# Performance work log

Hardware: AMD Instinct MI355X
Metric: run time of the kernel (lower is better)

The kernel has to match this reference:

```python
import jax, jax.numpy as jnp
import numpy as np

N_NODES = 100000


def gcn_conv(x, W, b, src, dst, num_nodes):
    """PyG GCNConv: add self-loops, symmetric deg^{-1/2} normalization,
    linear transform, scatter-add aggregation (source -> target), bias."""
    h = x @ W  # [N, out]
    # degree on target nodes, counting the added self-loop (+1)
    deg = jax.ops.segment_sum(jnp.ones_like(dst, dtype=h.dtype), dst,
                              num_segments=num_nodes) + 1.0
    dinv = jax.lax.rsqrt(deg)  # deg >= 1 always
    norm = dinv[src] * dinv[dst]  # [E]
    agg = jax.ops.segment_sum(h[src] * norm[:, None], dst,
                              num_segments=num_nodes)
    # self-loop contribution: norm_ii = dinv[i]^2
    out = agg + h * (dinv * dinv)[:, None]
    return out + b


def setup_inputs() -> dict:
    key = jax.random.key(0)
    ks = jax.random.split(key, 8)
    num_features, hidden, emb = 64, 64, 32
    x = jax.random.normal(ks[0], (N_NODES, num_features), dtype=jnp.float32)
    edge_index = jax.random.randint(ks[1], (2, 1600000), 0, N_NODES, dtype=jnp.int64)
    def glorot(k, shape):
        lim = float(np.sqrt(6.0 / (shape[0] + shape[1])))
        return jax.random.uniform(k, shape, jnp.float32, -lim, lim)
    return {
        "x": x,
        "edge_index": edge_index,
        "W1": glorot(ks[2], (num_features, hidden)),
        "b1": jnp.zeros((hidden,), jnp.float32),
        "W2": glorot(ks[3], (hidden, hidden)),
        "b2": jnp.zeros((hidden,), jnp.float32),
        "Wf": glorot(ks[4], (hidden, emb)),
        "bf": jnp.zeros((emb,), jnp.float32),
    }


def reference(x, edge_index, W1, b1, W2, b2, Wf, bf):
    src, dst = edge_index[0], edge_index[1]
    n = x.shape[0]
    h = gcn_conv(x, W1, b1, src, dst, n)
    h = jax.nn.relu(h)  # dropout is identity in eval mode
    h = gcn_conv(h, W2, b2, src, dst, n)
    h = jax.nn.relu(h)
    return h @ Wf + bf
```

## Files before the change

### kernel.cpp

```cpp
#include <hip/hip_runtime.h>


#define NODE_SHIFT 8
#define NODES_PER_BKT 256
#define BKT_CAP 5120
#define CSR_CAP 7168
#define NB_PART 256
#define HPAD 68

__device__ __forceinline__ unsigned short f2bf_rne(float f) {
    unsigned int u = __float_as_uint(f);
    unsigned int r = (u + 0x7FFFu + ((u >> 16) & 1u)) >> 16;
    return (unsigned short)r;
}
__device__ __forceinline__ float bf_lo(unsigned int u) {
    return __uint_as_float(u << 16);
}
__device__ __forceinline__ float bf_hi(unsigned int u) {
    return __uint_as_float(u & 0xFFFF0000u);
}

__global__ __launch_bounds__(256) void partition_kernel(const int* __restrict__ src,
                                                        const int* __restrict__ dst, int E,
                                                        int* __restrict__ bkt_cursor,
                                                        unsigned int* __restrict__ staging,
                                                        int K1, int CHK) {
    __shared__ int lcnt[400];
    __shared__ int lcur[400];
    const int tid = threadIdx.x;
    const int start = blockIdx.x * CHK;
    const int end = min(E, start + CHK);
    for (int k = tid; k < 400; k += 256) lcnt[k] = 0;
    __syncthreads();
    const int s4 = start >> 2;
    const int e4 = end >> 2;
    for (int i = s4 + tid; i < e4; i += 256) {
        const int4 d = ((const int4*)dst)[i];
        atomicAdd(&lcnt[d.x >> NODE_SHIFT], 1);
        atomicAdd(&lcnt[d.y >> NODE_SHIFT], 1);
        atomicAdd(&lcnt[d.z >> NODE_SHIFT], 1);
        atomicAdd(&lcnt[d.w >> NODE_SHIFT], 1);
    }
    __syncthreads();
    for (int k = tid; k < K1; k += 256) {
        int c = lcnt[k];
        int g = c ? atomicAdd(&bkt_cursor[k], c) : 0;
        lcur[k] = k * BKT_CAP + g;
    }
    __syncthreads();
    for (int i = s4 + tid; i < e4; i += 256) {
        const int4 d = ((const int4*)dst)[i];
        const int4 s = ((const int4*)src)[i];
        int pos;
        pos = atomicAdd(&lcur[d.x >> NODE_SHIFT], 1);
        staging[pos] = ((unsigned int)(d.x & (NODES_PER_BKT - 1)) << 17) | (unsigned int)s.x;
        pos = atomicAdd(&lcur[d.y >> NODE_SHIFT], 1);
        staging[pos] = ((unsigned int)(d.y & (NODES_PER_BKT - 1)) << 17) | (unsigned int)s.y;
        pos = atomicAdd(&lcur[d.z >> NODE_SHIFT], 1);
        staging[pos] = ((unsigned int)(d.z & (NODES_PER_BKT - 1)) << 17) | (unsigned int)s.z;
        pos = atomicAdd(&lcur[d.w >> NODE_SHIFT], 1);
        staging[pos] = ((unsigned int)(d.w & (NODES_PER_BKT - 1)) << 17) | (unsigned int)s.w;
    }
}

__global__ __launch_bounds__(256) void bucket_build_kernel(const unsigned int* __restrict__ staging,
                                                           const int* __restrict__ bkt_cursor,
                                                           float* __restrict__ dinv,
                                                           int* __restrict__ offs,
                                                           int* __restrict__ n_e,
                                                           int* __restrict__ csr_src,
                                                           int N) {
    __shared__ int cnt[NODES_PER_BKT];
    __shared__ int wsum[4];
    const int tid = threadIdx.x;
    const int node0 = blockIdx.x * NODES_PER_BKT;
    const int estart = blockIdx.x * BKT_CAP;
    const int eend = estart + bkt_cursor[blockIdx.x];
    const int cstart = blockIdx.x * CSR_CAP;

    cnt[tid] = 0;
    __syncthreads();
    for (int e = estart + tid; e < eend; e += 256)
        atomicAdd(&cnt[staging[e] >> 17], 1);
    __syncthreads();

    const int lane = tid & 63;
    const int wave = tid >> 6;
    const int c = cnt[tid];
    const int cp = (c + 7) & ~7;
    int inc = cp;
#pragma unroll
    for (int o = 1; o < 64; o <<= 1) {
        int t = __shfl_up(inc, o, 64);
        if (lane >= o) inc += t;
    }
    if (lane == 63) wsum[wave] = inc;
    __syncthreads();
    int wpre = 0;
#pragma unroll
    for (int w = 0; w < 4; w++) wpre += (w < wave) ? wsum[w] : 0;
    const int p = cstart + wpre + inc - cp;

    const int node = node0 + tid;
    __syncthreads();
    if (node < N) {
        offs[node] = p;
        n_e[node] = cp;
        dinv[node] = rsqrtf((float)c + 1.0f);
    }
    cnt[tid] = p;
    __syncthreads();
    for (int e = estart + tid; e < eend; e += 256) {
        const unsigned int r = staging[e];
        int pos = atomicAdd(&cnt[r >> 17], 1);
        csr_src[pos] = (int)(r & 0x1FFFFu);
    }
    for (int j = c; j < cp; j++) csr_src[p + j] = N;
}

__global__ __launch_bounds__(256) void gemm1_kernel(const float* __restrict__ X,
                                                    const float* __restrict__ W,
                                                    const float* __restrict__ dinv,
                                                    unsigned short* __restrict__ Y, int N) {
    constexpr int OUTC = 64, RPT = 8;
    constexpr int R = 128;
    constexpr int RPAD = R + (R / 32) * 4;
    __shared__ float Ws[64 * OUTC];
    __shared__ float Xt[64 * RPAD];

    const int tid = threadIdx.x;
    const int row0 = blockIdx.x * R;

    for (int l = tid; l < 64 * OUTC / 4; l += 256)
        ((float4*)Ws)[l] = ((const float4*)W)[l];

    for (int l = tid; l < R * 16; l += 256) {
        const int r = l & (R - 1);
        const int kq = l >> 7;
        float4 v = make_float4(0.f, 0.f, 0.f, 0.f);
        const int row = row0 + r;
        if (row < N) v = ((const float4*)(X + (long)row * 64))[kq];
        const int rp = r + (r >> 5) * 4;
        Xt[(4 * kq + 0) * RPAD + rp] = v.x;
        Xt[(4 * kq + 1) * RPAD + rp] = v.y;
        Xt[(4 * kq + 2) * RPAD + rp] = v.z;
        Xt[(4 * kq + 3) * RPAD + rp] = v.w;
    }
    __syncthreads();

    const int cg = tid % 16;
    const int rg = tid / 16;
    const int c0 = cg * 4;
    const int r0 = rg * RPT;
    const int r0p = r0 + (r0 >> 5) * 4;

    float acc[RPT][4];
#pragma unroll
    for (int i = 0; i < RPT; i++)
#pragma unroll
        for (int j = 0; j < 4; j++) acc[i][j] = 0.f;

#pragma unroll 4
    for (int k = 0; k < 64; k++) {
        float xv[RPT];
        const float4 xa = *(const float4*)&Xt[k * RPAD + r0p];
        const float4 xb = *(const float4*)&Xt[k * RPAD + r0p + 4];
        xv[0] = xa.x; xv[1] = xa.y; xv[2] = xa.z; xv[3] = xa.w;
        xv[4] = xb.x; xv[5] = xb.y; xv[6] = xb.z; xv[7] = xb.w;
        const float4 wa = *(const float4*)&Ws[k * OUTC + c0];
        const float wv[4] = {wa.x, wa.y, wa.z, wa.w};
#pragma unroll
        for (int i = 0; i < RPT; i++)
#pragma unroll
            for (int j = 0; j < 4; j++)
                acc[i][j] += xv[i] * wv[j];
    }

#pragma unroll
    for (int i = 0; i < RPT; i++) {
        const int row = row0 + r0 + i;
        if (row < N) {
            const float sc = dinv[row];
            ushort4 o16;
            o16.x = f2bf_rne(acc[i][0] * sc);
            o16.y = f2bf_rne(acc[i][1] * sc);
            o16.z = f2bf_rne(acc[i][2] * sc);
            o16.w = f2bf_rne(acc[i][3] * sc);
            *(ushort4*)&Y[(long)row * OUTC + c0] = o16;
        }
    }
}

template <int OUTC, bool HEAD>
__global__ __launch_bounds__(256) void fused_agg_gemm_kernel(
    const unsigned short* __restrict__ T, const int* __restrict__ offs,
    const int* __restrict__ n_e, const int* __restrict__ csr_src,
    const float* __restrict__ dinv, const float* __restrict__ aggbias,
    const float* __restrict__ W, const float* __restrict__ headbias,
    void* __restrict__ Yv, int N) {
    __shared__ float Ws[2048];
    __shared__ float hs[32 * HPAD];

    const int tid = threadIdx.x;
    constexpr int KSPLIT = (OUTC == 64) ? 32 : 64;

    for (int l = tid; l < 512; l += 256)
        ((float4*)Ws)[l] = ((const float4*)W)[l];

    const int nl = tid >> 3;
    const int node = blockIdx.x * 32 + nl;
    const int l8 = tid & 7;
    const int fo = l8 * 8;

    float o[8];
    if (node < N) {
        const int start = offs[node];
        const int n_edges = n_e[node];
        const int* ep = csr_src + start;

        float acc[8];
#pragma unroll
        for (int j = 0; j < 8; j++) acc[j] = 0.f;

        if (n_edges > 0) {
            int4 ia = ((const int4*)ep)[0];
            int4 ib = ((const int4*)ep)[1];
            for (int e = 0; e < n_edges; e += 8) {
                uint4 h[8];
                h[0] = *(const uint4*)&T[(long)ia.x * 64 + fo];
                h[1] = *(const uint4*)&T[(long)ia.y * 64 + fo];
                h[2] = *(const uint4*)&T[(long)ia.z * 64 + fo];
                h[3] = *(const uint4*)&T[(long)ia.w * 64 + fo];
                h[4] = *(const uint4*)&T[(long)ib.x * 64 + fo];
                h[5] = *(const uint4*)&T[(long)ib.y * 64 + fo];
                h[6] = *(const uint4*)&T[(long)ib.z * 64 + fo];
                h[7] = *(const uint4*)&T[(long)ib.w * 64 + fo];
                const int next = e + 8;
                if (next < n_edges) {
                    ia = ((const int4*)(ep + next))[0];
                    ib = ((const int4*)(ep + next))[1];
                }
#pragma unroll
                for (int j = 0; j < 8; j++) {
                    acc[0] += bf_lo(h[j].x); acc[1] += bf_hi(h[j].x);
                    acc[2] += bf_lo(h[j].y); acc[3] += bf_hi(h[j].y);
                    acc[4] += bf_lo(h[j].z); acc[5] += bf_hi(h[j].z);
                    acc[6] += bf_lo(h[j].w); acc[7] += bf_hi(h[j].w);
                }
            }
        }

        const float di = dinv[node];
        const uint4 sv = *(const uint4*)&T[(long)node * 64 + fo];
        const float self[8] = {bf_lo(sv.x), bf_hi(sv.x), bf_lo(sv.y), bf_hi(sv.y),
                               bf_lo(sv.z), bf_hi(sv.z), bf_lo(sv.w), bf_hi(sv.w)};
        const float4 ba = *(const float4*)&aggbias[fo];
        const float4 bb = *(const float4*)&aggbias[fo + 4];
        const float bv[8] = {ba.x, ba.y, ba.z, ba.w, bb.x, bb.y, bb.z, bb.w};
#pragma unroll
        for (int j = 0; j < 8; j++)
            o[j] = fmaxf(di * (acc[j] + self[j]) + bv[j], 0.f);
    } else {
#pragma unroll
        for (int j = 0; j < 8; j++) o[j] = 0.f;
    }
    float* hp = &hs[nl * HPAD + fo];
    *(float4*)hp = make_float4(o[0], o[1], o[2], o[3]);
    *(float4*)(hp + 4) = make_float4(o[4], o[5], o[6], o[7]);
    __syncthreads();

    constexpr int CPT = OUTC / 8;
    const int row = blockIdx.x * 32 + (tid >> 3);
    const int c0 = (tid & 7) * CPT;
    const int lrow = tid >> 3;

    float acc2[CPT];
#pragma unroll
    for (int j = 0; j < CPT; j++) acc2[j] = 0.f;

#pragma unroll 4
    for (int k = 0; k < KSPLIT; k++) {
        const float x = hs[lrow * HPAD + k];
        const float4 wa = *(const float4*)&Ws[k * OUTC + c0];
        acc2[0] += x * wa.x;
        acc2[1] += x * wa.y;
        acc2[2] += x * wa.z;
        acc2[3] += x * wa.w;
        if (CPT == 8) {
            const float4 wb = *(const float4*)&Ws[k * OUTC + c0 + 4];
            acc2[4] += x * wb.x;
            acc2[5] += x * wb.y;
            acc2[6] += x * wb.z;
            acc2[7] += x * wb.w;
        }
    }

    if (OUTC == 64) {
        __syncthreads();
        for (int l = tid; l < 512; l += 256)
            ((float4*)Ws)[l] = ((const float4*)W)[512 + l];
        __syncthreads();
#pragma unroll 4
        for (int k = 32; k < 64; k++) {
            const float x = hs[lrow * HPAD + k];
            const float4 wa = *(const float4*)&Ws[(k - 32) * OUTC + c0];
            acc2[0] += x * wa.x;
            acc2[1] += x * wa.y;
            acc2[2] += x * wa.z;
            acc2[3] += x * wa.w;
            const float4 wb = *(const float4*)&Ws[(k - 32) * OUTC + c0 + 4];
            acc2[4] += x * wb.x;
            acc2[5] += x * wb.y;
            acc2[6] += x * wb.z;
            acc2[7] += x * wb.w;
        }
    }

    if (row < N) {
        if (HEAD) {
            const float4 hb = *(const float4*)&headbias[c0];
            float* yp = &((float*)Yv)[(long)row * OUTC + c0];
            *(float4*)yp = make_float4(acc2[0] + hb.x, acc2[1] + hb.y,
                                       acc2[2] + hb.z, acc2[3] + hb.w);
        } else {
            const float sc = dinv[row];
            unsigned short* yp = &((unsigned short*)Yv)[(long)row * OUTC + c0];
            ushort4 o0, o1;
            o0.x = f2bf_rne(acc2[0] * sc); o0.y = f2bf_rne(acc2[1] * sc);
            o0.z = f2bf_rne(acc2[2] * sc); o0.w = f2bf_rne(acc2[3] * sc);
            o1.x = f2bf_rne(acc2[4] * sc); o1.y = f2bf_rne(acc2[5] * sc);
            o1.z = f2bf_rne(acc2[6] * sc); o1.w = f2bf_rne(acc2[7] * sc);
            *(ushort4*)yp = o0;
            *(ushort4*)(yp + 4) = o1;
        }
    }
}

extern "C" void kernel_launch(void* const* d_in, const int* in_sizes, int n_in,
                              void* d_out, int out_size, void* d_ws, size_t ws_size,
                              hipStream_t stream) {
    const float* x  = (const float*)d_in[0];
    const int*   ei = (const int*)d_in[1];
    const float* W1 = (const float*)d_in[2];
    const float* b1 = (const float*)d_in[3];
    const float* W2 = (const float*)d_in[4];
    const float* b2 = (const float*)d_in[5];
    const float* Wf = (const float*)d_in[6];
    const float* bf = (const float*)d_in[7];

    const int N = in_sizes[0] / 64;
    const int E = in_sizes[1] / 2;
    const int* src = ei;
    const int* dst = ei + E;
    const int K1 = (N + NODES_PER_BKT - 1) / NODES_PER_BKT;

    char* ws = (char*)d_ws;
    size_t off = 0;
    auto alloc = [&](size_t bytes) -> void* {
        void* p = ws + off;
        off = (off + bytes + 255) & ~(size_t)255;
        return p;
    };
    int*   bkt_cursor  = (int*)alloc(512 * 4);
    float* dinv        = (float*)alloc((size_t)N * 4);
    int*   offs        = (int*)alloc((size_t)N * 4);
    int*   n_e         = (int*)alloc((size_t)N * 4);
    unsigned int* staging = (unsigned int*)alloc((size_t)K1 * BKT_CAP * 4);
    int*   csr_src     = (int*)alloc((size_t)K1 * CSR_CAP * 4);
    unsigned short* A  = (unsigned short*)alloc(((size_t)N + 1) * 64 * 2);
    unsigned short* A2 = (unsigned short*)alloc(((size_t)N + 1) * 64 * 2);

    const int NB = NB_PART;
    const int CHK = ((E / 4 + NB - 1) / NB) * 4;

    hipMemsetAsync(bkt_cursor, 0, (size_t)K1 * 4, stream);
    hipMemsetAsync(A + (size_t)N * 64, 0, 128, stream);
    hipMemsetAsync(A2 + (size_t)N * 64, 0, 128, stream);
    partition_kernel<<<NB, 256, 0, stream>>>(src, dst, E, bkt_cursor, staging, K1, CHK);
    bucket_build_kernel<<<K1, 256, 0, stream>>>(staging, bkt_cursor, dinv, offs, n_e, csr_src, N);

    gemm1_kernel<<<(N + 127) / 128, 256, 0, stream>>>(x, W1, dinv, A, N);

    fused_agg_gemm_kernel<64, false><<<(N + 31) / 32, 256, 0, stream>>>(
        A, offs, n_e, csr_src, dinv, b1, W2, nullptr, A2, N);

    fused_agg_gemm_kernel<32, true><<<(N + 31) / 32, 256, 0, stream>>>(
        A2, offs, n_e, csr_src, dinv, b2, Wf, bf, d_out, N);
}
```

Measured before the change: 213.2 us.

## Halve bucket size to 128 nodes and fold padding-row memsets into kernels

Buckets shrink from 256 to 128 nodes, which doubles the number of bucket_build blocks (about 782 instead of 391) and the partition blocks (512), so the CSR build gets more parallelism. The block-local scan is adapted to 128 active threads while the blocks stay at 256. The two hipMemsetAsync calls that zero the padding row are removed, and that zeroing is done inside gemm1 and the first fused kernel instead, which saves launches. The risk is that bucket overflow now has less slack (BKT_CAP 2560 for a mean of about 2048 edges), and the partition kernel's local histogram grows to 800 entries.

```diff
diff --git a/kernel.cpp b/kernel.cpp
--- a/kernel.cpp
+++ b/kernel.cpp
@@ -1,11 +1,11 @@
 #include <hip/hip_runtime.h>
 
 
-#define NODE_SHIFT 8
-#define NODES_PER_BKT 256
-#define BKT_CAP 5120
-#define CSR_CAP 7168
-#define NB_PART 256
+#define NODE_SHIFT 7
+#define NODES_PER_BKT 128
+#define BKT_CAP 2560
+#define CSR_CAP 3072
+#define NB_PART 512
 #define HPAD 68
 
 __device__ __forceinline__ unsigned short f2bf_rne(float f) {
@@ -25,12 +25,12 @@
                                                         int* __restrict__ bkt_cursor,
                                                         unsigned int* __restrict__ staging,
                                                         int K1, int CHK) {
-    __shared__ int lcnt[400];
-    __shared__ int lcur[400];
+    __shared__ int lcnt[800];
+    __shared__ int lcur[800];
     const int tid = threadIdx.x;
     const int start = blockIdx.x * CHK;
     const int end = min(E, start + CHK);
-    for (int k = tid; k < 400; k += 256) lcnt[k] = 0;
+    for (int k = tid; k < 800; k += 256) lcnt[k] = 0;
     __syncthreads();
     const int s4 = start >> 2;
     const int e4 = end >> 2;
@@ -71,51 +71,54 @@
                                                            int* __restrict__ csr_src,
                                                            int N) {
     __shared__ int cnt[NODES_PER_BKT];
-    __shared__ int wsum[4];
+    __shared__ int wsum[2];
     const int tid = threadIdx.x;
     const int node0 = blockIdx.x * NODES_PER_BKT;
     const int estart = blockIdx.x * BKT_CAP;
     const int eend = estart + bkt_cursor[blockIdx.x];
     const int cstart = blockIdx.x * CSR_CAP;
 
-    cnt[tid] = 0;
+    if (tid < NODES_PER_BKT) cnt[tid] = 0;
     __syncthreads();
     for (int e = estart + tid; e < eend; e += 256)
         atomicAdd(&cnt[staging[e] >> 17], 1);
     __syncthreads();
 
-    const int lane = tid & 63;
-    const int wave = tid >> 6;
-    const int c = cnt[tid];
-    const int cp = (c + 7) & ~7;
-    int inc = cp;
-#pragma unroll
-    for (int o = 1; o < 64; o <<= 1) {
-        int t = __shfl_up(inc, o, 64);
-        if (lane >= o) inc += t;
-    }
-    if (lane == 63) wsum[wave] = inc;
-    __syncthreads();
-    int wpre = 0;
-#pragma unroll
-    for (int w = 0; w < 4; w++) wpre += (w < wave) ? wsum[w] : 0;
-    const int p = cstart + wpre + inc - cp;
-
-    const int node = node0 + tid;
-    __syncthreads();
-    if (node < N) {
-        offs[node] = p;
-        n_e[node] = cp;
-        dinv[node] = rsqrtf((float)c + 1.0f);
-    }
-    cnt[tid] = p;
+    int c = 0, cp = 0, p = 0;
+    if (tid < NODES_PER_BKT) {
+        const int lane = tid & 63;
+        const int wave = tid >> 6;
+        c = cnt[tid];
+        cp = (c + 7) & ~7;
+        int inc = cp;
+#pragma unroll
+        for (int o = 1; o < 64; o <<= 1) {
+            int t = __shfl_up(inc, o, 64);
+            if (lane >= o) inc += t;
+        }
+        if (lane == 63) wsum[wave] = inc;
+        __syncthreads();
+        const int wpre = (wave == 1) ? wsum[0] : 0;
+        p = cstart + wpre + inc - cp;
+        const int node = node0 + tid;
+        if (node < N) {
+            offs[node] = p;
+            n_e[node] = cp;
+            dinv[node] = rsqrtf((float)c + 1.0f);
+        }
+    } else {
+        __syncthreads();
+    }
+    __syncthreads();
+    if (tid < NODES_PER_BKT) cnt[tid] = p;
     __syncthreads();
     for (int e = estart + tid; e < eend; e += 256) {
         const unsigned int r = staging[e];
         int pos = atomicAdd(&cnt[r >> 17], 1);
         csr_src[pos] = (int)(r & 0x1FFFFu);
     }
-    for (int j = c; j < cp; j++) csr_src[p + j] = N;
+    if (tid < NODES_PER_BKT)
+        for (int j = c; j < cp; j++) csr_src[p + j] = N;
 }
 
 __global__ __launch_bounds__(256) void gemm1_kernel(const float* __restrict__ X,
@@ -130,6 +133,11 @@
 
     const int tid = threadIdx.x;
     const int row0 = blockIdx.x * R;
+
+    if (blockIdx.x == 0 && tid < 16) {
+        ushort4 z = {0, 0, 0, 0};
+        *(ushort4*)&Y[(long)N * 64 + tid * 4] = z;
+    }
 
     for (int l = tid; l < 64 * OUTC / 4; l += 256)
         ((float4*)Ws)[l] = ((const float4*)W)[l];
@@ -203,6 +211,11 @@
 
     const int tid = threadIdx.x;
     constexpr int KSPLIT = (OUTC == 64) ? 32 : 64;
+
+    if (!HEAD && blockIdx.x == 0 && tid < 16) {
+        ushort4 z = {0, 0, 0, 0};
+        *(ushort4*)&((unsigned short*)Yv)[(long)N * 64 + tid * 4] = z;
+    }
 
     for (int l = tid; l < 512; l += 256)
         ((float4*)Ws)[l] = ((const float4*)W)[l];
@@ -361,7 +374,7 @@
         off = (off + bytes + 255) & ~(size_t)255;
         return p;
     };
-    int*   bkt_cursor  = (int*)alloc(512 * 4);
+    int*   bkt_cursor  = (int*)alloc(1024 * 4);
     float* dinv        = (float*)alloc((size_t)N * 4);
     int*   offs        = (int*)alloc((size_t)N * 4);
     int*   n_e         = (int*)alloc((size_t)N * 4);
@@ -374,8 +387,6 @@
     const int CHK = ((E / 4 + NB - 1) / NB) * 4;
 
     hipMemsetAsync(bkt_cursor, 0, (size_t)K1 * 4, stream);
-    hipMemsetAsync(A + (size_t)N * 64, 0, 128, stream);
-    hipMemsetAsync(A2 + (size_t)N * 64, 0, 128, stream);
     partition_kernel<<<NB, 256, 0, stream>>>(src, dst, E, bkt_cursor, staging, K1, CHK);
     bucket_build_kernel<<<K1, 256, 0, stream>>>(staging, bkt_cursor, dinv, offs, n_e, csr_src, N);
 
```

New measurement: 217.2 us. About the same (+1.9%).
